# Kernel tuning notes

Measured on AMD Instinct MI355X. Metric: run time of the kernel, lower is better.

The kernel has to match this reference:

```python
import jax, jax.numpy as jnp
import numpy as np

DIM = 384
HEADS = 12
WIN = (7, 7)
N = WIN[0] * WIN[1]
B = 4096
NW = 64  # number of windows sharing one mask


def _relative_position_index(win):
    wh, ww = win
    coords = np.stack(np.meshgrid(np.arange(wh), np.arange(ww), indexing='ij'))  # (2,wh,ww)
    flat = coords.reshape(2, -1)                                                 # (2, N)
    rel = flat[:, :, None] - flat[:, None, :]                                    # (2, N, N)
    rel = rel.transpose(1, 2, 0).astype(np.int64)
    rel[:, :, 0] += wh - 1
    rel[:, :, 1] += ww - 1
    rel[:, :, 0] *= 2 * ww - 1
    return jnp.asarray(rel.sum(-1), dtype=jnp.int32)                             # (N, N)


def setup_inputs() -> dict:
    key = jax.random.key(0)
    ks = jax.random.split(key, 7)
    std = 0.02
    return {
        'x': jax.random.normal(ks[0], (B, N, DIM), jnp.float32),
        'mask': jax.random.normal(ks[1], (NW, N, N), jnp.float32),
        'qkv_w': jax.random.normal(ks[2], (3 * DIM, DIM), jnp.float32) * std,
        'qkv_b': jnp.zeros((3 * DIM,), jnp.float32),
        'bias_table': jax.random.normal(ks[3], ((2 * WIN[0] - 1) * (2 * WIN[1] - 1), HEADS), jnp.float32) * std,
        'proj_w': jax.random.normal(ks[4], (DIM, DIM), jnp.float32) * std,
        'proj_b': jnp.zeros((DIM,), jnp.float32),
        'rel_idx': _relative_position_index(WIN),
    }


def reference(x, mask, qkv_w, qkv_b, bias_table, proj_w, proj_b, rel_idx):
    B_, n, c = x.shape
    h = HEADS
    d = c // h
    scale = d ** -0.5

    qkv = x @ qkv_w.T + qkv_b                                  # (B_, N, 3C)
    qkv = qkv.reshape(B_, n, 3, h, d).transpose(2, 0, 3, 1, 4)  # (3, B_, H, N, D)
    q, k, v = qkv[0], qkv[1], qkv[2]

    attn = jnp.einsum('bhnd,bhmd->bhnm', q, k) * scale          # (B_, H, N, N)

    bias = bias_table[rel_idx]                                  # (N, N, H)
    attn = attn + bias.transpose(2, 0, 1)[None]                 # add (1, H, N, N)

    nW = mask.shape[0]
    attn = attn.reshape(B_ // nW, nW, h, n, n) + mask[None, :, None]
    attn = attn.reshape(B_, h, n, n)

    attn = jax.nn.softmax(attn, axis=-1)
    out = jnp.einsum('bhnm,bhmd->bhnd', attn, v)                # (B_, H, N, D)
    out = out.transpose(0, 2, 1, 3).reshape(B_, n, c)
    return out @ proj_w.T + proj_b
```

## Files before the change

### kernel.cpp

```cpp
#include <hip/hip_runtime.h>

typedef __bf16 bf16;
typedef __bf16 bf16x4 __attribute__((ext_vector_type(4)));
typedef __bf16 bf16x8 __attribute__((ext_vector_type(8)));
typedef float f32x4 __attribute__((ext_vector_type(4)));
typedef float f32x16 __attribute__((ext_vector_type(16)));
typedef int i32x2 __attribute__((ext_vector_type(2)));
typedef unsigned int u32;

#define DIMC 384
#define NHEADS 12
#define NTOK 49
#define NWINB 4096
#define MROWS (NWINB*NTOK)

#define MFMA32(A,B,C) __builtin_amdgcn_mfma_f32_32x32x16_bf16(A,B,C,0,0,0)

__global__ __launch_bounds__(256) void k_convert(const float4* __restrict__ in,
                                                 bf16x4* __restrict__ out, int n4) {
  int stride = gridDim.x * blockDim.x;
  for (int i = blockIdx.x * blockDim.x + threadIdx.x; i < n4; i += stride) {
    float4 v = in[i];
    bf16x4 o;
    o[0] = (bf16)v.x; o[1] = (bf16)v.y; o[2] = (bf16)v.z; o[3] = (bf16)v.w;
    out[i] = o;
  }
}

__global__ __launch_bounds__(256) void k_biasT(const float* __restrict__ table,
                                               const int* __restrict__ rel,
                                               float* __restrict__ outp) {
  int i = blockIdx.x * 256 + threadIdx.x;
  if (i < NHEADS * NTOK * NTOK) {
    int h = i / (NTOK * NTOK), r2 = i - h * (NTOK * NTOK);
    int key = r2 / NTOK, q = r2 - key * NTOK;
    outp[i] = table[rel[q * NTOK + key] * NHEADS + h];
  }
}

__global__ __launch_bounds__(256) void k_maskT(const float* __restrict__ mask,
                                               float* __restrict__ outp) {
  int i = blockIdx.x * 256 + threadIdx.x;
  if (i < 64 * NTOK * NTOK) {
    int w = i / (NTOK * NTOK), r2 = i - w * (NTOK * NTOK);
    int key = r2 / NTOK, q = r2 - key * NTOK;
    outp[i] = mask[(w * NTOK + q) * NTOK + key];
  }
}

template <int MODE>
__global__ __launch_bounds__(256) void k_gemm(const bf16* __restrict__ A,
                                              const bf16* __restrict__ Bw,
                                              const float* __restrict__ bias,
                                              bf16* __restrict__ oQ, bf16* __restrict__ oK,
                                              bf16* __restrict__ oV, float* __restrict__ oP) {
  constexpr int LDT = 72;
  __shared__ __align__(16) bf16 lA[128 * LDT];
  __shared__ __align__(16) bf16 lB[128 * LDT];
  const int t = threadIdx.x;
  const int l = t & 63;
  const int wv = t >> 6;
  const int wr = wv >> 1, wc = wv & 1;
  const int m0 = blockIdx.x * 128;
  const int n0 = blockIdx.y * 128;
  const int lr = l & 15, lg = l >> 4;

  f32x4 acc[4][4] = {};

  for (int k0 = 0; k0 < DIMC; k0 += 64) {
    __syncthreads();
#pragma unroll
    for (int i = 0; i < 4; ++i) {
      int idx = i * 256 + t;
      int row = idx >> 3;
      int col = (idx & 7) * 8;
      *reinterpret_cast<bf16x8*>(&lA[row * LDT + col]) =
          *reinterpret_cast<const bf16x8*>(&A[(m0 + row) * DIMC + k0 + col]);
      *reinterpret_cast<bf16x8*>(&lB[row * LDT + col]) =
          *reinterpret_cast<const bf16x8*>(&Bw[(n0 + row) * DIMC + k0 + col]);
    }
    __syncthreads();
#pragma unroll
    for (int kk = 0; kk < 64; kk += 32) {
      bf16x8 af[4], bfv[4];
#pragma unroll
      for (int f = 0; f < 4; ++f)
        af[f] = *reinterpret_cast<const bf16x8*>(&lA[(wr * 64 + f * 16 + lr) * LDT + kk + lg * 8]);
#pragma unroll
      for (int f = 0; f < 4; ++f)
        bfv[f] = *reinterpret_cast<const bf16x8*>(&lB[(wc * 64 + f * 16 + lr) * LDT + kk + lg * 8]);
#pragma unroll
      for (int fm = 0; fm < 4; ++fm)
#pragma unroll
        for (int fn = 0; fn < 4; ++fn)
          acc[fm][fn] = __builtin_amdgcn_mfma_f32_16x16x32_bf16(af[fm], bfv[fn], acc[fm][fn], 0, 0, 0);
    }
  }

#pragma unroll
  for (int fm = 0; fm < 4; ++fm) {
#pragma unroll
    for (int fn = 0; fn < 4; ++fn) {
      int c = n0 + wc * 64 + fn * 16 + lr;
      float bc = bias[c];
#pragma unroll
      for (int r = 0; r < 4; ++r) {
        int m = m0 + wr * 64 + fm * 16 + lg * 4 + r;
        float v = acc[fm][fn][r] + bc;
        if (MODE == 0) {
          int b = m / 49, n = m - b * 49;
          int which = c / 384;
          int rem = c - which * 384;
          int h = rem >> 5, d = rem & 31;
          bf16* dst = which == 0 ? oQ : (which == 1 ? oK : oV);
          dst[((b * 12 + h) * 49 + n) * 32 + d] = (bf16)v;
        } else {
          oP[m * 384 + c] = v;
        }
      }
    }
  }
}

__global__ __launch_bounds__(256, 4) void k_attn(const bf16* __restrict__ Q,
                                                 const bf16* __restrict__ K,
                                                 const bf16* __restrict__ V,
                                                 const float* __restrict__ biasT,
                                                 const float* __restrict__ maskT,
                                                 bf16* __restrict__ H) {
  __shared__ __align__(16) bf16 Vl[4][32 * 72];
  const int t = threadIdx.x, l = t & 63, wv = t >> 6;
  const int p = blockIdx.x * 4 + wv;
  const int b = p / 12, h = p - b * 12;
  const int w = b & 63;
  const size_t base = (size_t)p * (49 * 32);
  const int c = l & 31, b5 = l >> 5;
  bf16* vl = Vl[wv];

  {
    bf16x4 z = {};
    for (int i = l; i < 128; i += 64) {
      int d = i >> 2, kq = 48 + (i & 3) * 4;
      *reinterpret_cast<bf16x4*>(&vl[d * 72 + kq]) = z;
    }
  }
  for (int i = l; i < 392; i += 64) {
    int key = i >> 3, dc = (i & 7) * 4;
    bf16x4 vv = *reinterpret_cast<const bf16x4*>(&V[base + key * 32 + dc]);
#pragma unroll
    for (int j = 0; j < 4; ++j) vl[(dc + j) * 72 + key] = vv[j];
  }

  bf16x8 kf[2][2], qf[2][2];
#pragma unroll
  for (int f = 0; f < 2; ++f) {
    int row = f * 32 + c; if (row > 48) row = 48;
#pragma unroll
    for (int kd = 0; kd < 2; ++kd) {
      kf[f][kd] = *reinterpret_cast<const bf16x8*>(&K[base + row * 32 + kd * 16 + b5 * 8]);
      qf[f][kd] = *reinterpret_cast<const bf16x8*>(&Q[base + row * 32 + kd * 16 + b5 * 8]);
    }
  }

  const float scale = 0.17677669529663689f;
  const float* bT = biasT + h * 2401;
  const float* mT = maskT + w * 2401;
  const int qq =  c;

#pragma unroll
  for (int fn = 0; fn < 2; ++fn) {
    f32x16 s0 = {}, s1 = {};
    s0 = MFMA32(kf[0][0], qf[fn][0], s0);
    s0 = MFMA32(kf[0][1], qf[fn][1], s0);
    s1 = MFMA32(kf[1][0], qf[fn][0], s1);
    s1 = MFMA32(kf[1][1], qf[fn][1], s1);

    int q = fn * 32 + qq;
    int qc = q > 48 ? 48 : q;

    float vals[32];
    float vmax = -1e30f;
#pragma unroll
    for (int fm = 0; fm < 2; ++fm) {
#pragma unroll
      for (int r = 0; r < 16; ++r) {
        int kb = fm * 32 + (r & 3) + 8 * (r >> 2);
        int key = kb + 4 * b5;
        float sv = fm ? s1[r] : s0[r];
        float v;
        if (key < 49) {
          float cm = bT[key * 49 + qc] + mT[key * 49 + qc];
          v = fmaf(sv, scale, cm);
        } else {
          v = -1e30f;
        }
        vals[fm * 16 + r] = v;
        vmax = fmaxf(vmax, v);
      }
    }
    vmax = fmaxf(vmax, __shfl_xor(vmax, 32));
    float sum = 0.f;
#pragma unroll
    for (int i = 0; i < 32; ++i) {
      float e = __expf(vals[i] - vmax);
      vals[i] = e;
      sum += e;
    }
    sum += __shfl_xor(sum, 32);
    float inv = 1.f / sum;

    f32x16 o = {};
#pragma unroll
    for (int kk = 0; kk < 4; ++kk) {
      int ib = (kk >> 1) * 16 + 8 * (kk & 1);
      union { bf16 hh[2]; u32 u; } cv;
      u32 A0, A1, B0, B1;
      cv.hh[0] = (bf16)(vals[ib + 0] * inv); cv.hh[1] = (bf16)(vals[ib + 1] * inv); A0 = cv.u;
      cv.hh[0] = (bf16)(vals[ib + 2] * inv); cv.hh[1] = (bf16)(vals[ib + 3] * inv); A1 = cv.u;
      cv.hh[0] = (bf16)(vals[ib + 4] * inv); cv.hh[1] = (bf16)(vals[ib + 5] * inv); B0 = cv.u;
      cv.hh[0] = (bf16)(vals[ib + 6] * inv); cv.hh[1] = (bf16)(vals[ib + 7] * inv); B1 = cv.u;
      i32x2 sw0 = __builtin_amdgcn_permlane32_swap((int)A0, (int)B0, false, false);
      i32x2 sw1 = __builtin_amdgcn_permlane32_swap((int)A1, (int)B1, false, false);
      union { u32 d[4]; bf16x8 v8; } pa;
      pa.d[0] = (u32)sw0[0]; pa.d[1] = (u32)sw1[0];
      pa.d[2] = (u32)sw0[1]; pa.d[3] = (u32)sw1[1];
      bf16x8 vf = *reinterpret_cast<const bf16x8*>(&vl[c * 72 + kk * 16 + b5 * 8]);
      o = MFMA32(pa.v8, vf, o);
    }

#pragma unroll
    for (int r = 0; r < 16; ++r) {
      int qrow = fn * 32 + (r & 3) + 8 * (r >> 2) + 4 * b5;
      if (qrow < 49)
        H[((size_t)b * 49 + qrow) * 384 + h * 32 + c] = (bf16)o[r];
    }
  }
}

extern "C" void kernel_launch(void* const* d_in, const int* in_sizes, int n_in,
                              void* d_out, int out_size, void* d_ws, size_t ws_size,
                              hipStream_t stream) {
  const float* x     = (const float*)d_in[0];
  const float* mask  = (const float*)d_in[1];
  const float* qkvw  = (const float*)d_in[2];
  const float* qkvb  = (const float*)d_in[3];
  const float* btab  = (const float*)d_in[4];
  const float* projw = (const float*)d_in[5];
  const float* projb = (const float*)d_in[6];
  const int*   rel   = (const int*)d_in[7];
  float* out = (float*)d_out;

  const size_t NELEM = (size_t)MROWS * DIMC;
  char* ws = (char*)d_ws;
  bf16*  xb    = (bf16*)ws;
  bf16*  vb    = (bf16*)(ws + 154140672);
  float* biasT = (float*)(ws + 308281344);
  bf16*  wqkv  = (bf16*)(ws + 308396800);
  float* maskT = (float*)(ws + 308396800);
  bf16*  wproj = (bf16*)(ws + 309281536);
  bf16* qb = (bf16*)d_out;
  bf16* kb = qb + NELEM;

  k_convert<<<2048, 256, 0, stream>>>((const float4*)x, (bf16x4*)xb, (int)(NELEM / 4));
  k_convert<<<432, 256, 0, stream>>>((const float4*)qkvw, (bf16x4*)wqkv, 3 * DIMC * DIMC / 4);
  k_convert<<<144, 256, 0, stream>>>((const float4*)projw, (bf16x4*)wproj, DIMC * DIMC / 4);
  k_biasT<<<(NHEADS * NTOK * NTOK + 255) / 256, 256, 0, stream>>>(btab, rel, biasT);

  k_gemm<0><<<dim3(MROWS / 128, 1152 / 128), 256, 0, stream>>>(xb, wqkv, qkvb, qb, kb, vb, nullptr);
  k_maskT<<<(64 * NTOK * NTOK + 255) / 256, 256, 0, stream>>>(mask, maskT);
  k_attn<<<(NWINB * NHEADS) / 4, 256, 0, stream>>>(qb, kb, vb, biasT, maskT, xb);
  k_gemm<1><<<dim3(MROWS / 128, 384 / 128), 256, 0, stream>>>(xb, wproj, projb, nullptr, nullptr, nullptr, out);
}
```

Before: 851.6 us.

## Use direct global-to-LDS loads with XOR swizzle and N-major block order in GEMM

New measurement: 893.2 us. +4.9%, slower.

```diff
diff --git a/kernel.cpp b/kernel.cpp
--- a/kernel.cpp
+++ b/kernel.cpp
@@ -15,6 +15,11 @@
 #define MROWS (NWINB*NTOK)
 
 #define MFMA32(A,B,C) __builtin_amdgcn_mfma_f32_32x32x16_bf16(A,B,C,0,0,0)
+
+#define GLOAD16(gsrc, lbase) \
+  __builtin_amdgcn_global_load_lds( \
+      (const __attribute__((address_space(1))) u32*)(gsrc), \
+      (__attribute__((address_space(3))) u32*)(lbase), 16, 0, 0)
 
 __global__ __launch_bounds__(256) void k_convert(const float4* __restrict__ in,
                                                  bf16x4* __restrict__ out, int n4) {
@@ -54,16 +59,18 @@
                                               const float* __restrict__ bias,
                                               bf16* __restrict__ oQ, bf16* __restrict__ oK,
                                               bf16* __restrict__ oV, float* __restrict__ oP) {
-  constexpr int LDT = 72;
-  __shared__ __align__(16) bf16 lA[128 * LDT];
-  __shared__ __align__(16) bf16 lB[128 * LDT];
+  __shared__ __align__(16) bf16 lA[128 * 64];
+  __shared__ __align__(16) bf16 lB[128 * 64];
   const int t = threadIdx.x;
   const int l = t & 63;
   const int wv = t >> 6;
   const int wr = wv >> 1, wc = wv & 1;
-  const int m0 = blockIdx.x * 128;
-  const int n0 = blockIdx.y * 128;
+  const int n0 = blockIdx.x * 128;
+  const int m0 = blockIdx.y * 128;
   const int lr = l & 15, lg = l >> 4;
+
+  const int srow = wv * 32 + (l >> 3);
+  const int scolb = (l & 7) * 16;
 
   f32x4 acc[4][4] = {};
 
@@ -71,24 +78,29 @@
     __syncthreads();
 #pragma unroll
     for (int i = 0; i < 4; ++i) {
-      int idx = i * 256 + t;
-      int row = idx >> 3;
-      int col = (idx & 7) * 8;
-      *reinterpret_cast<bf16x8*>(&lA[row * LDT + col]) =
-          *reinterpret_cast<const bf16x8*>(&A[(m0 + row) * DIMC + k0 + col]);
-      *reinterpret_cast<bf16x8*>(&lB[row * LDT + col]) =
-          *reinterpret_cast<const bf16x8*>(&Bw[(n0 + row) * DIMC + k0 + col]);
+      int row = srow + i * 8;
+      int scol = (scolb ^ ((row & 7) << 4)) >> 1;
+      GLOAD16(&A[(size_t)(m0 + row) * DIMC + k0 + scol], &lA[wv * 2048 + i * 512]);
+      GLOAD16(&Bw[(size_t)(n0 + row) * DIMC + k0 + scol], &lB[wv * 2048 + i * 512]);
     }
     __syncthreads();
 #pragma unroll
     for (int kk = 0; kk < 64; kk += 32) {
       bf16x8 af[4], bfv[4];
 #pragma unroll
-      for (int f = 0; f < 4; ++f)
-        af[f] = *reinterpret_cast<const bf16x8*>(&lA[(wr * 64 + f * 16 + lr) * LDT + kk + lg * 8]);
-#pragma unroll
-      for (int f = 0; f < 4; ++f)
-        bfv[f] = *reinterpret_cast<const bf16x8*>(&lB[(wc * 64 + f * 16 + lr) * LDT + kk + lg * 8]);
+      for (int f = 0; f < 4; ++f) {
+        int row = wr * 64 + f * 16 + lr;
+        int cb = (kk + lg * 8) * 2;
+        af[f] = *reinterpret_cast<const bf16x8*>(
+            &lA[row * 64 + ((cb ^ ((row & 7) << 4)) >> 1)]);
+      }
+#pragma unroll
+      for (int f = 0; f < 4; ++f) {
+        int row = wc * 64 + f * 16 + lr;
+        int cb = (kk + lg * 8) * 2;
+        bfv[f] = *reinterpret_cast<const bf16x8*>(
+            &lB[row * 64 + ((cb ^ ((row & 7) << 4)) >> 1)]);
+      }
 #pragma unroll
       for (int fm = 0; fm < 4; ++fm)
 #pragma unroll
@@ -165,7 +177,6 @@
   const float scale = 0.17677669529663689f;
   const float* bT = biasT + h * 2401;
   const float* mT = maskT + w * 2401;
-  const int qq =  c;
 
 #pragma unroll
   for (int fn = 0; fn < 2; ++fn) {
@@ -175,7 +186,7 @@
     s1 = MFMA32(kf[1][0], qf[fn][0], s1);
     s1 = MFMA32(kf[1][1], qf[fn][1], s1);
 
-    int q = fn * 32 + qq;
+    int q = fn * 32 + c;
     int qc = q > 48 ? 48 : q;
 
     float vals[32];
@@ -184,8 +195,7 @@
     for (int fm = 0; fm < 2; ++fm) {
 #pragma unroll
       for (int r = 0; r < 16; ++r) {
-        int kb = fm * 32 + (r & 3) + 8 * (r >> 2);
-        int key = kb + 4 * b5;
+        int key = fm * 32 + (r & 3) + 8 * (r >> 2) + 4 * b5;
         float sv = fm ? s1[r] : s0[r];
         float v;
         if (key < 49) {
@@ -266,8 +276,8 @@
   k_convert<<<144, 256, 0, stream>>>((const float4*)projw, (bf16x4*)wproj, DIMC * DIMC / 4);
   k_biasT<<<(NHEADS * NTOK * NTOK + 255) / 256, 256, 0, stream>>>(btab, rel, biasT);
 
-  k_gemm<0><<<dim3(MROWS / 128, 1152 / 128), 256, 0, stream>>>(xb, wqkv, qkvb, qb, kb, vb, nullptr);
+  k_gemm<0><<<dim3(1152 / 128, MROWS / 128), 256, 0, stream>>>(xb, wqkv, qkvb, qb, kb, vb, nullptr);
   k_maskT<<<(64 * NTOK * NTOK + 255) / 256, 256, 0, stream>>>(mask, maskT);
   k_attn<<<(NWINB * NHEADS) / 4, 256, 0, stream>>>(qb, kb, vb, biasT, maskT, xb);
-  k_gemm<1><<<dim3(MROWS / 128, 384 / 128), 256, 0, stream>>>(xb, wproj, projb, nullptr, nullptr, nullptr, out);
-}
+  k_gemm<1><<<dim3(384 / 128, MROWS / 128), 256, 0, stream>>>(xb, wproj, projb, nullptr, nullptr, nullptr, out);
+}
```
